# Kernel optimization log

Measured on AMD Instinct MI355X. Metric: run time of the kernel, lower is better.

Reference implementation:

```python
import jax, jax.numpy as jnp
import numpy as np

DIM = 1024
HID = 256
MAXT = 2048
B = 4
T = 2048


def setup_inputs() -> dict:
    key = jax.random.key(0)
    ks = jax.random.split(key, 10)
    s_in = 1.0 / np.sqrt(DIM)   # keeps K ~ N(0,1) so exp(K) is stable
    s_h = 1.0 / np.sqrt(HID)
    # xavier-uniform bound for square wbias: sqrt(6/(T+T))
    wb_bound = float(np.sqrt(6.0 / (MAXT + MAXT)))
    return {
        "x": jax.random.normal(ks[0], (B, T, DIM), dtype=jnp.float32),
        "Wq": jax.random.normal(ks[1], (DIM, HID), dtype=jnp.float32) * s_in,
        "bq": jnp.zeros((HID,), dtype=jnp.float32),
        "Wk": jax.random.normal(ks[2], (DIM, HID), dtype=jnp.float32) * s_in,
        "bk": jnp.zeros((HID,), dtype=jnp.float32),
        "Wv": jax.random.normal(ks[3], (DIM, HID), dtype=jnp.float32) * s_in,
        "bv": jnp.zeros((HID,), dtype=jnp.float32),
        "Wp": jax.random.normal(ks[4], (HID, DIM), dtype=jnp.float32) * s_h,
        "bp": jnp.zeros((DIM,), dtype=jnp.float32),
        "wbias": jax.random.uniform(ks[5], (MAXT, MAXT), dtype=jnp.float32,
                                    minval=-wb_bound, maxval=wb_bound),
    }


def reference(x, Wq, bq, Wk, bk, Wv, bv, Wp, bp, wbias):
    Bn, Tn, _ = x.shape
    Q = x @ Wq + bq            # [B,T,H]
    K = x @ Wk + bk            # [B,T,H]
    V = x @ Wv + bv            # [B,T,H]
    ew = jnp.exp(wbias[:Tn, :Tn])          # [T,T]
    eK = jnp.exp(K)                         # [B,T,H]
    num = jnp.einsum('ts,bsh->bth', ew, eK * V)   # [B,T,H]
    den = jnp.einsum('ts,bsh->bth', ew, eK)       # [B,T,H]
    Yt = jax.nn.sigmoid(Q) * (num / den)          # [B,T,H]
    return Yt @ Wp + bp                            # [B,T,DIM]
```

## Files before the change

kernel.cpp:

```cpp
#include <hip/hip_runtime.h>
#include <hip/hip_bf16.h>


#define T_   2048
#define DIM_ 1024
#define HID_ 256
#define B_   4

typedef __attribute__((ext_vector_type(8))) short bf16x8;
typedef __attribute__((ext_vector_type(4))) float f32x4;

static __device__ __forceinline__ unsigned short f2b(float f) {
  __hip_bfloat16 h = __float2bfloat16(f);
  return __builtin_bit_cast(unsigned short, h);
}

static __device__ __forceinline__ void gld16(const void* g, const void* l) {
  __builtin_amdgcn_global_load_lds((const __attribute__((address_space(1))) void*)g,
                                   (__attribute__((address_space(3))) void*)l, 16, 0, 0);
}

__global__ __launch_bounds__(256) void gemm_bt(
    const unsigned short* __restrict__ A,
    const unsigned short* __restrict__ Bt,
    float* __restrict__ C,
    const float* __restrict__ bias,
    int M, int N, int K)
{
  __shared__ unsigned short As[128 * 32];
  __shared__ unsigned short Bs[128 * 32];
  const int tid  = threadIdx.x;
  const int lane = tid & 63;
  const int wave = tid >> 6;
  const int wr = wave >> 1, wc = wave & 1;
  const long bm = (long)blockIdx.y * 128;
  const long bn = (long)blockIdx.x * 128;

  const int srow = tid >> 2;
  const int sk   = (tid & 3) * 8;
  const unsigned short* ap0 = A  + (bm + srow)      * (long)K + sk;
  const unsigned short* ap1 = A  + (bm + srow + 64) * (long)K + sk;
  const unsigned short* bp0 = Bt + (bn + srow)      * (long)K + sk;
  const unsigned short* bp1 = Bt + (bn + srow + 64) * (long)K + sk;

  char* AsB = (char*)As;
  char* BsB = (char*)Bs;
  char* ldsA0 = AsB + wave * 1024;
  char* ldsA1 = AsB + 4096 + wave * 1024;
  char* ldsB0 = BsB + wave * 1024;
  char* ldsB1 = BsB + 4096 + wave * 1024;

  f32x4 acc[4][4] = {};

  const int fr  = lane & 15;
  const int fkb = (lane >> 4) * 16;

  const int nk = K >> 5;
  for (int kt = 0; kt < nk; ++kt) {
    gld16(ap0, ldsA0);
    gld16(ap1, ldsA1);
    gld16(bp0, ldsB0);
    gld16(bp1, ldsB1);
    ap0 += 32; ap1 += 32; bp0 += 32; bp1 += 32;
    asm volatile("s_waitcnt vmcnt(0)" ::: "memory");
    __syncthreads();

    bf16x8 av[4], bv[4];
#pragma unroll
    for (int m = 0; m < 4; ++m)
      av[m] = *(const bf16x8*)(AsB + (wr * 64 + m * 16 + fr) * 64 + fkb);
#pragma unroll
    for (int n = 0; n < 4; ++n)
      bv[n] = *(const bf16x8*)(BsB + (wc * 64 + n * 16 + fr) * 64 + fkb);
#pragma unroll
    for (int m = 0; m < 4; ++m)
#pragma unroll
      for (int n = 0; n < 4; ++n)
        acc[m][n] = __builtin_amdgcn_mfma_f32_16x16x32_bf16(av[m], bv[n], acc[m][n], 0, 0, 0);
    __syncthreads();
  }

  const long crow0 = bm + wr * 64 + ((lane >> 4) << 2);
  const long ccol0 = bn + wc * 64 + fr;
#pragma unroll
  for (int n = 0; n < 4; ++n) {
    const long col = ccol0 + n * 16;
    const float bb = bias ? bias[col] : 0.f;
#pragma unroll
    for (int m = 0; m < 4; ++m) {
#pragma unroll
      for (int r = 0; r < 4; ++r) {
        C[(crow0 + m * 16 + r) * (long)N + col] = acc[m][n][r] + bb;
      }
    }
  }
}

__global__ void convert_f2b(const float4* __restrict__ in, ushort4* __restrict__ out,
                            int n4, int doExp) {
  int i = blockIdx.x * blockDim.x + threadIdx.x;
  if (i >= n4) return;
  float4 v = in[i];
  if (doExp) { v.x = __expf(v.x); v.y = __expf(v.y); v.z = __expf(v.z); v.w = __expf(v.w); }
  ushort4 o;
  o.x = f2b(v.x); o.y = f2b(v.y); o.z = f2b(v.z); o.w = f2b(v.w);
  out[i] = o;
}

__global__ void convert_w(const float* __restrict__ Wq, const float* __restrict__ Wk,
                          const float* __restrict__ Wv, const float* __restrict__ bq,
                          const float* __restrict__ bk, const float* __restrict__ bv,
                          const float* __restrict__ Wp,
                          unsigned short* __restrict__ WqkvT,
                          unsigned short* __restrict__ WpT,
                          float* __restrict__ biascat) {
  int idx = blockIdx.x * 256 + threadIdx.x;
  if (idx < 768 * 1024) {
    int n = idx >> 10, k = idx & 1023;
    const float* W = (n < 256) ? Wq : (n < 512) ? Wk : Wv;
    WqkvT[idx] = f2b(W[k * 256 + (n & 255)]);
  }
  if (idx < 1024 * 256) {
    int d = idx >> 8, h = idx & 255;
    WpT[idx] = f2b(Wp[h * 1024 + d]);
  }
  if (idx < 768) {
    const float* bb = (idx < 256) ? bq : (idx < 512) ? bk : bv;
    biascat[idx] = bb[idx & 255];
  }
}

__global__ void elt1_kernel(const float* __restrict__ C1, unsigned short* __restrict__ B2T) {
  __shared__ unsigned short ekT[64][65];
  __shared__ unsigned short ekvT[64][65];
  const int h0 = blockIdx.x * 64;
  const int s0 = blockIdx.y * 64;
  const int b  = blockIdx.z;
  const int t  = threadIdx.x;
#pragma unroll
  for (int i = 0; i < 16; ++i) {
    int idx = i * 256 + t;
    int si = idx >> 6, hi = idx & 63;
    const float* base = C1 + (long)(b * T_ + s0 + si) * 768;
    float k = base[256 + h0 + hi];
    float v = base[512 + h0 + hi];
    float ek = __expf(k);
    ekT[hi][si]  = f2b(ek);
    ekvT[hi][si] = f2b(ek * v);
  }
  __syncthreads();
#pragma unroll
  for (int i = 0; i < 16; ++i) {
    int idx = i * 256 + t;
    int hi = idx >> 6, si = idx & 63;
    B2T[(long)(b * 512 + h0 + hi) * 2048 + s0 + si]       = ekvT[hi][si];
    B2T[(long)(b * 512 + 256 + h0 + hi) * 2048 + s0 + si] = ekT[hi][si];
  }
}

__global__ void elt2_kernel(const float* __restrict__ C1, const float* __restrict__ C2,
                            unsigned short* __restrict__ Yt) {
  int idx = blockIdx.x * 256 + threadIdx.x;
  int h = idx & 255, m = idx >> 8;
  int b = m >> 11, tt = m & 2047;
  float q   = C1[(long)m * 768 + h];
  float num = C2[(long)tt * 2048 + b * 512 + h];
  float den = C2[(long)tt * 2048 + b * 512 + 256 + h];
  float sig = 1.f / (1.f + __expf(-q));
  Yt[idx] = f2b(sig * num / den);
}

extern "C" void kernel_launch(void* const* d_in, const int* in_sizes, int n_in,
                              void* d_out, int out_size, void* d_ws, size_t ws_size,
                              hipStream_t stream) {
  const float* x     = (const float*)d_in[0];
  const float* Wq    = (const float*)d_in[1];
  const float* bq    = (const float*)d_in[2];
  const float* Wk    = (const float*)d_in[3];
  const float* bk    = (const float*)d_in[4];
  const float* Wv    = (const float*)d_in[5];
  const float* bv    = (const float*)d_in[6];
  const float* Wp    = (const float*)d_in[7];
  const float* bp    = (const float*)d_in[8];
  const float* wbias = (const float*)d_in[9];

  char* ws = (char*)d_ws;
  unsigned short* xb    = (unsigned short*)(ws + 0);
  float*          C2    = (float*)(ws + 0);
  unsigned short* WqkvT = (unsigned short*)(ws + 16777216);
  unsigned short* WpT   = (unsigned short*)(ws + 18350080);
  float*          biascat = (float*)(ws + 18874368);
  unsigned short* ewb   = (unsigned short*)(ws + 18878464);
  unsigned short* Yt    = (unsigned short*)(ws + 18878464);
  float*          C1    = (float*)(ws + 27267072);
  unsigned short* B2T   = (unsigned short*)(ws + 52432896);
  float*          out   = (float*)d_out;

  convert_f2b<<<8192, 256, 0, stream>>>((const float4*)x, (ushort4*)xb, 2097152, 0);
  convert_f2b<<<4096, 256, 0, stream>>>((const float4*)wbias, (ushort4*)ewb, 1048576, 1);
  convert_w<<<3072, 256, 0, stream>>>(Wq, Wk, Wv, bq, bk, bv, Wp, WqkvT, WpT, biascat);

  gemm_bt<<<dim3(6, 64), 256, 0, stream>>>(xb, WqkvT, C1, biascat, 8192, 768, 1024);
  elt1_kernel<<<dim3(4, 32, 4), 256, 0, stream>>>(C1, B2T);
  gemm_bt<<<dim3(16, 16), 256, 0, stream>>>(ewb, B2T, C2, nullptr, 2048, 2048, 2048);
  elt2_kernel<<<8192, 256, 0, stream>>>(C1, C2, Yt);
  gemm_bt<<<dim3(8, 64), 256, 0, stream>>>(Yt, WpT, out, bp, 8192, 1024, 256);
}
```

Measured before the change: 221.2 us.

## Add split-K and narrower tiles to GEMMs, fuse prep conversions into one kernel

Templates the GEMM on the N tile width so some calls use 128x64 tiles, which doubles the block count and gives small-N GEMMs better occupancy across the many CUs. When the workspace is large enough, it adds a split-K path for the 2048-cube GEMM that writes two partial slices, and the elt2 kernel sums them. The three conversion kernels are merged into one launch to cut launch overhead. The cost is extra C2 memory traffic for the split-K partials, plus a workspace-size dependent code path.

```diff
diff --git a/kernel.cpp b/kernel.cpp
--- a/kernel.cpp
+++ b/kernel.cpp
@@ -20,28 +20,30 @@
                                    (__attribute__((address_space(3))) void*)l, 16, 0, 0);
 }
 
+template <int BN>
 __global__ __launch_bounds__(256) void gemm_bt(
     const unsigned short* __restrict__ A,
     const unsigned short* __restrict__ Bt,
     float* __restrict__ C,
     const float* __restrict__ bias,
-    int M, int N, int K)
+    int M, int N, int K, int Ksub)
 {
   __shared__ unsigned short As[128 * 32];
-  __shared__ unsigned short Bs[128 * 32];
+  __shared__ unsigned short Bs[BN * 32];
   const int tid  = threadIdx.x;
   const int lane = tid & 63;
   const int wave = tid >> 6;
   const int wr = wave >> 1, wc = wave & 1;
   const long bm = (long)blockIdx.y * 128;
-  const long bn = (long)blockIdx.x * 128;
+  const long bn = (long)blockIdx.x * BN;
+  const long kbase = (long)blockIdx.z * Ksub;
 
   const int srow = tid >> 2;
   const int sk   = (tid & 3) * 8;
-  const unsigned short* ap0 = A  + (bm + srow)      * (long)K + sk;
-  const unsigned short* ap1 = A  + (bm + srow + 64) * (long)K + sk;
-  const unsigned short* bp0 = Bt + (bn + srow)      * (long)K + sk;
-  const unsigned short* bp1 = Bt + (bn + srow + 64) * (long)K + sk;
+  const unsigned short* ap0 = A  + (bm + srow) * (long)K + kbase + sk;
+  const unsigned short* ap1 = ap0 + 64 * (long)K;
+  const unsigned short* bp0 = Bt + (bn + srow) * (long)K + kbase + sk;
+  const unsigned short* bp1 = bp0 + 64 * (long)K;
 
   char* AsB = (char*)As;
   char* BsB = (char*)Bs;
@@ -50,83 +52,92 @@
   char* ldsB0 = BsB + wave * 1024;
   char* ldsB1 = BsB + 4096 + wave * 1024;
 
-  f32x4 acc[4][4] = {};
+  constexpr int NF = BN / 32;
+  f32x4 acc[4][NF] = {};
 
   const int fr  = lane & 15;
   const int fkb = (lane >> 4) * 16;
 
-  const int nk = K >> 5;
+  const int nk = Ksub >> 5;
   for (int kt = 0; kt < nk; ++kt) {
     gld16(ap0, ldsA0);
     gld16(ap1, ldsA1);
     gld16(bp0, ldsB0);
-    gld16(bp1, ldsB1);
-    ap0 += 32; ap1 += 32; bp0 += 32; bp1 += 32;
+    if constexpr (BN == 128) gld16(bp1, ldsB1);
+    ap0 += 32; ap1 += 32; bp0 += 32;
+    if constexpr (BN == 128) bp1 += 32;
     asm volatile("s_waitcnt vmcnt(0)" ::: "memory");
     __syncthreads();
 
-    bf16x8 av[4], bv[4];
+    bf16x8 av[4], bv[NF];
 #pragma unroll
     for (int m = 0; m < 4; ++m)
       av[m] = *(const bf16x8*)(AsB + (wr * 64 + m * 16 + fr) * 64 + fkb);
 #pragma unroll
-    for (int n = 0; n < 4; ++n)
-      bv[n] = *(const bf16x8*)(BsB + (wc * 64 + n * 16 + fr) * 64 + fkb);
+    for (int n = 0; n < NF; ++n)
+      bv[n] = *(const bf16x8*)(BsB + (wc * (BN / 2) + n * 16 + fr) * 64 + fkb);
 #pragma unroll
     for (int m = 0; m < 4; ++m)
 #pragma unroll
-      for (int n = 0; n < 4; ++n)
+      for (int n = 0; n < NF; ++n)
         acc[m][n] = __builtin_amdgcn_mfma_f32_16x16x32_bf16(av[m], bv[n], acc[m][n], 0, 0, 0);
     __syncthreads();
   }
 
+  float* Cz = C + (long)blockIdx.z * M * (long)N;
   const long crow0 = bm + wr * 64 + ((lane >> 4) << 2);
-  const long ccol0 = bn + wc * 64 + fr;
-#pragma unroll
-  for (int n = 0; n < 4; ++n) {
+  const long ccol0 = bn + wc * (BN / 2) + fr;
+#pragma unroll
+  for (int n = 0; n < NF; ++n) {
     const long col = ccol0 + n * 16;
     const float bb = bias ? bias[col] : 0.f;
 #pragma unroll
     for (int m = 0; m < 4; ++m) {
 #pragma unroll
       for (int r = 0; r < 4; ++r) {
-        C[(crow0 + m * 16 + r) * (long)N + col] = acc[m][n][r] + bb;
+        Cz[(crow0 + m * 16 + r) * (long)N + col] = acc[m][n][r] + bb;
       }
     }
   }
 }
 
-__global__ void convert_f2b(const float4* __restrict__ in, ushort4* __restrict__ out,
-                            int n4, int doExp) {
-  int i = blockIdx.x * blockDim.x + threadIdx.x;
-  if (i >= n4) return;
-  float4 v = in[i];
-  if (doExp) { v.x = __expf(v.x); v.y = __expf(v.y); v.z = __expf(v.z); v.w = __expf(v.w); }
-  ushort4 o;
-  o.x = f2b(v.x); o.y = f2b(v.y); o.z = f2b(v.z); o.w = f2b(v.w);
-  out[i] = o;
-}
-
-__global__ void convert_w(const float* __restrict__ Wq, const float* __restrict__ Wk,
-                          const float* __restrict__ Wv, const float* __restrict__ bq,
-                          const float* __restrict__ bk, const float* __restrict__ bv,
-                          const float* __restrict__ Wp,
-                          unsigned short* __restrict__ WqkvT,
-                          unsigned short* __restrict__ WpT,
-                          float* __restrict__ biascat) {
-  int idx = blockIdx.x * 256 + threadIdx.x;
-  if (idx < 768 * 1024) {
-    int n = idx >> 10, k = idx & 1023;
-    const float* W = (n < 256) ? Wq : (n < 512) ? Wk : Wv;
-    WqkvT[idx] = f2b(W[k * 256 + (n & 255)]);
-  }
-  if (idx < 1024 * 256) {
-    int d = idx >> 8, h = idx & 255;
-    WpT[idx] = f2b(Wp[h * 1024 + d]);
-  }
-  if (idx < 768) {
-    const float* bb = (idx < 256) ? bq : (idx < 512) ? bk : bv;
-    biascat[idx] = bb[idx & 255];
+__global__ void prep_kernel(const float* __restrict__ x, const float* __restrict__ wbias,
+                            const float* __restrict__ Wq, const float* __restrict__ Wk,
+                            const float* __restrict__ Wv, const float* __restrict__ bq,
+                            const float* __restrict__ bk, const float* __restrict__ bv,
+                            const float* __restrict__ Wp,
+                            unsigned short* __restrict__ xb, unsigned short* __restrict__ ewb,
+                            unsigned short* __restrict__ WqkvT, unsigned short* __restrict__ WpT,
+                            float* __restrict__ biascat) {
+  const int bid = blockIdx.x;
+  const int t = threadIdx.x;
+  if (bid < 8192) {
+    int i = bid * 256 + t;
+    float4 v = ((const float4*)x)[i];
+    ushort4 o; o.x = f2b(v.x); o.y = f2b(v.y); o.z = f2b(v.z); o.w = f2b(v.w);
+    ((ushort4*)xb)[i] = o;
+  } else if (bid < 12288) {
+    int i = (bid - 8192) * 256 + t;
+    float4 v = ((const float4*)wbias)[i];
+    ushort4 o;
+    o.x = f2b(__expf(v.x)); o.y = f2b(__expf(v.y));
+    o.z = f2b(__expf(v.z)); o.w = f2b(__expf(v.w));
+    ((ushort4*)ewb)[i] = o;
+  } else {
+    int idx = (bid - 12288) * 256 + t;
+    if (idx < 768 * 1024) {
+      int n = idx >> 10, k = idx & 1023;
+      const float* W = (n < 256) ? Wq : (n < 512) ? Wk : Wv;
+      WqkvT[idx] = f2b(W[k * 256 + (n & 255)]);
+    }
+    if (idx < 1024 * 256) {
+      int d = idx >> 8, h = idx & 255;
+      WpT[idx] = f2b(Wp[h * 1024 + d]);
+    }
+    if (idx < 768) {
+      const float* bb = (idx < 256) ? bq : (idx < 512) ? bk : bv;
+      biascat[idx] = bb[idx & 255];
+    }
   }
 }
 
@@ -159,13 +170,19 @@
 }
 
 __global__ void elt2_kernel(const float* __restrict__ C1, const float* __restrict__ C2,
-                            unsigned short* __restrict__ Yt) {
+                            unsigned short* __restrict__ Yt, int nslices) {
   int idx = blockIdx.x * 256 + threadIdx.x;
   int h = idx & 255, m = idx >> 8;
   int b = m >> 11, tt = m & 2047;
+  long i_num = (long)tt * 2048 + b * 512 + h;
+  long i_den = i_num + 256;
   float q   = C1[(long)m * 768 + h];
-  float num = C2[(long)tt * 2048 + b * 512 + h];
-  float den = C2[(long)tt * 2048 + b * 512 + 256 + h];
+  float num = C2[i_num];
+  float den = C2[i_den];
+  if (nslices == 2) {
+    num += C2[i_num + 4194304];
+    den += C2[i_den + 4194304];
+  }
   float sig = 1.f / (1.f + __expf(-q));
   Yt[idx] = f2b(sig * num / den);
 }
@@ -185,24 +202,43 @@
   const float* wbias = (const float*)d_in[9];
 
   char* ws = (char*)d_ws;
-  unsigned short* xb    = (unsigned short*)(ws + 0);
-  float*          C2    = (float*)(ws + 0);
-  unsigned short* WqkvT = (unsigned short*)(ws + 16777216);
-  unsigned short* WpT   = (unsigned short*)(ws + 18350080);
-  float*          biascat = (float*)(ws + 18874368);
-  unsigned short* ewb   = (unsigned short*)(ws + 18878464);
-  unsigned short* Yt    = (unsigned short*)(ws + 18878464);
-  float*          C1    = (float*)(ws + 27267072);
-  unsigned short* B2T   = (unsigned short*)(ws + 52432896);
-  float*          out   = (float*)d_out;
-
-  convert_f2b<<<8192, 256, 0, stream>>>((const float4*)x, (ushort4*)xb, 2097152, 0);
-  convert_f2b<<<4096, 256, 0, stream>>>((const float4*)wbias, (ushort4*)ewb, 1048576, 1);
-  convert_w<<<3072, 256, 0, stream>>>(Wq, Wk, Wv, bq, bk, bv, Wp, WqkvT, WpT, biascat);
-
-  gemm_bt<<<dim3(6, 64), 256, 0, stream>>>(xb, WqkvT, C1, biascat, 8192, 768, 1024);
+  const bool big = ws_size >= 76021760ull;
+
+  unsigned short *xb, *WqkvT, *WpT, *ewb, *Yt, *B2T;
+  float *C1, *C2, *biascat;
+  if (big) {
+    xb      = (unsigned short*)(ws + 0);
+    WqkvT   = (unsigned short*)(ws + 16777216);
+    biascat = (float*)(ws + 18350080);
+    C2      = (float*)(ws + 0);
+    ewb     = (unsigned short*)(ws + 33554432);
+    Yt      = (unsigned short*)(ws + 33554432);
+    C1      = (float*)(ws + 41943040);
+    B2T     = (unsigned short*)(ws + 67108864);
+    WpT     = (unsigned short*)(ws + 75497472);
+  } else {
+    xb      = (unsigned short*)(ws + 0);
+    C2      = (float*)(ws + 0);
+    WqkvT   = (unsigned short*)(ws + 16777216);
+    WpT     = (unsigned short*)(ws + 18350080);
+    biascat = (float*)(ws + 18874368);
+    ewb     = (unsigned short*)(ws + 18878464);
+    Yt      = (unsigned short*)(ws + 18878464);
+    C1      = (float*)(ws + 27267072);
+    B2T     = (unsigned short*)(ws + 52432896);
+  }
+  float* out = (float*)d_out;
+
+  prep_kernel<<<15360, 256, 0, stream>>>(x, wbias, Wq, Wk, Wv, bq, bk, bv, Wp,
+                                         xb, ewb, WqkvT, WpT, biascat);
+
+  gemm_bt<64><<<dim3(12, 64, 1), 256, 0, stream>>>(xb, WqkvT, C1, biascat, 8192, 768, 1024, 1024);
   elt1_kernel<<<dim3(4, 32, 4), 256, 0, stream>>>(C1, B2T);
-  gemm_bt<<<dim3(16, 16), 256, 0, stream>>>(ewb, B2T, C2, nullptr, 2048, 2048, 2048);
-  elt2_kernel<<<8192, 256, 0, stream>>>(C1, C2, Yt);
-  gemm_bt<<<dim3(8, 64), 256, 0, stream>>>(Yt, WpT, out, bp, 8192, 1024, 256);
-}
+  if (big) {
+    gemm_bt<128><<<dim3(16, 16, 2), 256, 0, stream>>>(ewb, B2T, C2, nullptr, 2048, 2048, 2048, 1024);
+  } else {
+    gemm_bt<64><<<dim3(32, 16, 1), 256, 0, stream>>>(ewb, B2T, C2, nullptr, 2048, 2048, 2048, 2048);
+  }
+  elt2_kernel<<<8192, 256, 0, stream>>>(C1, C2, Yt, big ? 2 : 1);
+  gemm_bt<64><<<dim3(16, 64, 1), 256, 0, stream>>>(Yt, WpT, out, bp, 8192, 1024, 256, 256);
+}
```

After: 201.1 us. 1.1x faster.
